# Kernel optimization log

Hardware: AMD Instinct MI355X
Metric: run time of the kernel (lower is better)

## Reference

```python
import math
import jax, jax.numpy as jnp
import numpy as np

EMBED = 1024
INTERNAL = 1024  # EMBED // downsample_rate(=1)
HEADS = 16


def setup_inputs() -> dict:
    key = jax.random.key(0)
    ks = jax.random.split(key, 11)
    b, n, m = 2, 2048, 2048
    s = 1.0 / math.sqrt(EMBED)
    inp = {
        "q": jax.random.normal(ks[0], (b, n, EMBED), jnp.float32),
        "k": jax.random.normal(ks[1], (b, m, EMBED), jnp.float32),
        "v": jax.random.normal(ks[2], (b, m, EMBED), jnp.float32),
        # Linear params (torch Linear: y = x @ W.T + b); store as [in, out].
        "Wq": jax.random.normal(ks[3], (EMBED, INTERNAL), jnp.float32) * s,
        "bq": jax.random.normal(ks[4], (INTERNAL,), jnp.float32) * s,
        "Wk": jax.random.normal(ks[5], (EMBED, INTERNAL), jnp.float32) * s,
        "bk": jax.random.normal(ks[6], (INTERNAL,), jnp.float32) * s,
        "Wv": jax.random.normal(ks[7], (EMBED, INTERNAL), jnp.float32) * s,
        "bv": jax.random.normal(ks[8], (INTERNAL,), jnp.float32) * s,
        "Wo": jax.random.normal(ks[9], (INTERNAL, EMBED), jnp.float32) * s,
        "bo": jax.random.normal(ks[10], (EMBED,), jnp.float32) * s,
    }
    return inp


def _split_heads(x):  # [b, n, c] -> [b, h, n, c/h]
    b, n, c = x.shape
    return x.reshape(b, n, HEADS, c // HEADS).transpose(0, 2, 1, 3)


def reference(q, k, v, Wq, bq, Wk, bk, Wv, bv, Wo, bo):
    qh = _split_heads(q @ Wq + bq)
    kh = _split_heads(k @ Wk + bk)
    vh = _split_heads(v @ Wv + bv)
    c_per_head = kh.shape[-1]
    attn = jnp.einsum("bhnc,bhmc->bhnm", qh, kh) / math.sqrt(c_per_head)
    attn = jax.nn.softmax(attn, axis=-1)
    out = jnp.einsum("bhnm,bhmc->bhnc", attn, vh)
    b, h, n, ch = out.shape
    out = out.transpose(0, 2, 1, 3).reshape(b, n, h * ch)
    return out @ Wo + bo
```

## Files before the change

kernel.cpp:

```cpp
#include <hip/hip_runtime.h>

#define EMBED 1024
#define HEADS 16
#define DHEAD 64
#define BATCH 2
#define SEQ 2048
#define ROWS (BATCH*SEQ)
#define SZA (ROWS*EMBED)
#define SW (EMBED*EMBED)

typedef _Float16 f16;
typedef __attribute__((ext_vector_type(2))) __fp16 h16x2;
typedef __attribute__((ext_vector_type(4))) _Float16 f16x4;
typedef __attribute__((ext_vector_type(8))) _Float16 f16x8;
typedef __attribute__((ext_vector_type(4))) float f32x4;

__device__ __forceinline__ void gld16(const f16* g, f16* lds) {
  __builtin_amdgcn_global_load_lds(
      (const __attribute__((address_space(1))) void*)g,
      (__attribute__((address_space(3))) void*)lds, 16, 0, 0);
}

__global__ __launch_bounds__(256) void pre_kernel(
    const float* __restrict__ q, const float* __restrict__ k,
    const float* __restrict__ v, f16* __restrict__ qc,
    f16* __restrict__ kc, f16* __restrict__ vc,
    const float* __restrict__ w0, const float* __restrict__ w1,
    const float* __restrict__ w2, const float* __restrict__ w3,
    f16* __restrict__ o0, f16* __restrict__ o1,
    f16* __restrict__ o2, f16* __restrict__ o3) {
  __shared__ float tile[32][33];
  const int y = blockIdx.y;
  if (y < 3) {
    const float* in = y == 0 ? q : y == 1 ? k : v;
    f16* out       = y == 0 ? qc : y == 1 ? kc : vc;
    int i = blockIdx.x * 256 + threadIdx.x;
    float4 f = ((const float4* __restrict__)in)[i];
    union { f16 h[4]; short4 s4; } u;
    u.h[0] = (f16)f.x; u.h[1] = (f16)f.y; u.h[2] = (f16)f.z; u.h[3] = (f16)f.w;
    ((short4* __restrict__)out)[i] = u.s4;
    return;
  }
  const int x = blockIdx.x;
  const int z = x >> 10, by = (x >> 5) & 31, bx = x & 31;
  const float* in = z == 0 ? w0 : z == 1 ? w1 : z == 2 ? w2 : w3;
  f16* out       = z == 0 ? o0 : z == 1 ? o1 : z == 2 ? o2 : o3;
  int tx = threadIdx.x & 31, ty = threadIdx.x >> 5;
  #pragma unroll
  for (int i = 0; i < 32; i += 8)
    tile[ty + i][tx] = in[(by*32 + ty + i)*EMBED + bx*32 + tx];
  __syncthreads();
  #pragma unroll
  for (int i = 0; i < 32; i += 8)
    out[(bx*32 + ty + i)*EMBED + by*32 + tx] = (f16)tile[tx][ty + i];
}

__global__ __launch_bounds__(256) void gemm3_kernel(
    const f16* __restrict__ qc, const f16* __restrict__ kc, const f16* __restrict__ vc,
    const f16* __restrict__ Wqt, const f16* __restrict__ Wkt, const f16* __restrict__ Wvt,
    const float* __restrict__ bq, const float* __restrict__ bk, const float* __restrict__ bv,
    f16* __restrict__ Qp, f16* __restrict__ Kp, f16* __restrict__ Vtg) {
  __shared__ __align__(16) f16 As[128*32];
  __shared__ __align__(16) f16 Bs[128*32];
  const int z = blockIdx.y;
  const f16 *A, *Bt; const float* bias; f16* C;
  int mbase, nbase, N, biasrow;
  if (z == 0)      { A=qc;  Bt=Wqt; bias=bq; C=Qp;  mbase=(blockIdx.x&31)*128; nbase=(blockIdx.x>>5)*128; N=EMBED; biasrow=0; }
  else if (z == 1) { A=kc;  Bt=Wkt; bias=bk; C=Kp;  mbase=(blockIdx.x&31)*128; nbase=(blockIdx.x>>5)*128; N=EMBED; biasrow=0; }
  else             { A=Wvt; Bt=vc;  bias=bv; C=Vtg; mbase=(blockIdx.x&7)*128;  nbase=(blockIdx.x>>3)*128; N=ROWS;  biasrow=1; }
  const int K = EMBED;
  const int tid = threadIdx.x;
  const int wave = tid >> 6, lane = tid & 63;
  const int lg = lane >> 4, lr = lane & 15;
  const int wm = (wave >> 1) * 64, wn = (wave & 1) * 64;
  const int sr = lane >> 2, sc = (lane & 3) * 8;
  const f16* gA0 = A  + (size_t)(mbase + wave*16 + sr)*K + sc;
  const f16* gA1 = A  + (size_t)(mbase + 64 + wave*16 + sr)*K + sc;
  const f16* gB0 = Bt + (size_t)(nbase + wave*16 + sr)*K + sc;
  const f16* gB1 = Bt + (size_t)(nbase + 64 + wave*16 + sr)*K + sc;
  f16* lA0 = &As[(wave*16)*32];
  f16* lA1 = &As[(64 + wave*16)*32];
  f16* lB0 = &Bs[(wave*16)*32];
  f16* lB1 = &Bs[(64 + wave*16)*32];
  f32x4 acc[4][4] = {};
  for (int k0 = 0; k0 < K; k0 += 32) {
    __syncthreads();
    gld16(gA0 + k0, lA0);
    gld16(gA1 + k0, lA1);
    gld16(gB0 + k0, lB0);
    gld16(gB1 + k0, lB1);
    __syncthreads();
    f16x8 af[4], bf[4];
    #pragma unroll
    for (int mt = 0; mt < 4; mt++)
      af[mt] = *(const f16x8*)&As[(wm + mt*16 + lr)*32 + lg*8];
    #pragma unroll
    for (int nt = 0; nt < 4; nt++)
      bf[nt] = *(const f16x8*)&Bs[(wn + nt*16 + lr)*32 + lg*8];
    #pragma unroll
    for (int mt = 0; mt < 4; mt++)
      #pragma unroll
      for (int nt = 0; nt < 4; nt++)
        acc[mt][nt] = __builtin_amdgcn_mfma_f32_16x16x32_f16(af[mt], bf[nt], acc[mt][nt], 0, 0, 0);
  }
  #pragma unroll
  for (int mt = 0; mt < 4; mt++)
    #pragma unroll
    for (int nt = 0; nt < 4; nt++)
      #pragma unroll
      for (int i = 0; i < 4; i++) {
        int row = mbase + wm + mt*16 + lg*4 + i;
        int col = nbase + wn + nt*16 + lr;
        float val = acc[mt][nt][i] + (biasrow ? bias[row] : bias[col]);
        C[(size_t)row*N + col] = (f16)val;
      }
}

__global__ __launch_bounds__(256) void gemmo_kernel(
    const f16* __restrict__ A, const f16* __restrict__ Bt,
    const float* __restrict__ bias, float* __restrict__ Cf) {
  __shared__ __align__(16) f16 As[128*32];
  __shared__ __align__(16) f16 Bs[64*32];
  const int K = EMBED, N = EMBED;
  const int tid = threadIdx.x;
  const int wave = tid >> 6, lane = tid & 63;
  const int lg = lane >> 4, lr = lane & 15;
  const int mbase = blockIdx.x * 128, nbase = blockIdx.y * 64;
  const int wm = (wave >> 1) * 64, wn = (wave & 1) * 32;
  const int sr = wave*16 + (lane >> 2), sc = (lane & 3) * 8;
  const f16* gA0 = A  + (size_t)(mbase + sr)*K + sc;
  const f16* gA1 = A  + (size_t)(mbase + 64 + sr)*K + sc;
  const f16* gB  = Bt + (size_t)(nbase + sr)*K + sc;
  f16* lA0 = &As[(wave*16)*32];
  f16* lA1 = &As[(64 + wave*16)*32];
  f16* lB  = &Bs[(wave*16)*32];
  f32x4 acc[4][2] = {};
  for (int k0 = 0; k0 < K; k0 += 32) {
    __syncthreads();
    gld16(gA0 + k0, lA0);
    gld16(gA1 + k0, lA1);
    gld16(gB  + k0, lB);
    __syncthreads();
    f16x8 af[4], bf[2];
    #pragma unroll
    for (int mt = 0; mt < 4; mt++)
      af[mt] = *(const f16x8*)&As[(wm + mt*16 + lr)*32 + lg*8];
    #pragma unroll
    for (int nt = 0; nt < 2; nt++)
      bf[nt] = *(const f16x8*)&Bs[(wn + nt*16 + lr)*32 + lg*8];
    #pragma unroll
    for (int mt = 0; mt < 4; mt++)
      #pragma unroll
      for (int nt = 0; nt < 2; nt++)
        acc[mt][nt] = __builtin_amdgcn_mfma_f32_16x16x32_f16(af[mt], bf[nt], acc[mt][nt], 0, 0, 0);
  }
  #pragma unroll
  for (int mt = 0; mt < 4; mt++)
    #pragma unroll
    for (int nt = 0; nt < 2; nt++)
      #pragma unroll
      for (int i = 0; i < 4; i++) {
        int row = mbase + wm + mt*16 + lg*4 + i;
        int col = nbase + wn + nt*16 + lr;
        Cf[(size_t)row*N + col] = acc[mt][nt][i] + bias[col];
      }
}

__global__ __launch_bounds__(256, 2) void attn_kernel(
    const f16* __restrict__ Qp, const f16* __restrict__ Kp,
    const f16* __restrict__ Vt, f16* __restrict__ Ob) {
  __shared__ __align__(16) f16 Ks[4096];
  __shared__ __align__(16) f16 Vs[4096];
  const int tid = threadIdx.x;
  const int wave = tid >> 6, lane = tid & 63;
  const int lg = lane >> 4, lr = lane & 15;
  const int gid = blockIdx.x;
  const int bh  = (gid & 7)*4 + ((gid >> 3) & 3);
  const int qblk = gid >> 5;
  const int h = bh & 15, b = bh >> 4;
  const int q0 = qblk*128 + wave*32;
  const f16* Qh = Qp + (size_t)b*SEQ*EMBED + h*DHEAD;
  const f16* Kh = Kp + (size_t)b*SEQ*EMBED + h*DHEAD;
  const f16* Vh = Vt + (size_t)h*DHEAD*ROWS + (size_t)b*SEQ;

  const f16* kst[2]; const f16* vst[2]; f16* kdst[2]; f16* vdst[2];
  #pragma unroll
  for (int m = 0; m < 2; m++) {
    int sgrp = m*4 + wave;
    int srow = sgrp*8 + (lane >> 3);
    int sch  = (lane & 7) ^ (srow & 7);
    int prow = ((srow>>5)&1)*32 + ((srow>>4)&1)*4 + ((srow>>2)&3)*8 + (srow&3);
    kst[m] = Kh + (size_t)prow*EMBED + sch*8;
    vst[m] = Vh + (size_t)srow*ROWS + sch*8;
    kdst[m] = &Ks[sgrp*512];
    vdst[m] = &Vs[sgrp*512];
  }

  f16x8 qf[2][2];
  #pragma unroll
  for (int qb = 0; qb < 2; qb++)
    #pragma unroll
    for (int ds = 0; ds < 2; ds++)
      qf[qb][ds] = *(const f16x8*)&Qh[(size_t)(q0 + qb*16 + lr)*EMBED + ds*32 + lg*8];

  const int c0 = ((lg)     ^ (lr & 7)) * 8;
  const int c1 = ((4 + lg) ^ (lr & 7)) * 8;

  f32x4 o[4][2] = {};
  float ls[2] = {};
  const float SC = 0.18033688011f;

  for (int kt = 0; kt < SEQ; kt += 64) {
    __syncthreads();
    gld16(kst[0] + (size_t)kt*EMBED, kdst[0]);
    gld16(kst[1] + (size_t)kt*EMBED, kdst[1]);
    gld16(vst[0] + kt, vdst[0]);
    gld16(vst[1] + kt, vdst[1]);
    __syncthreads();

    f16x8 ka[4][2];
    #pragma unroll
    for (int nb = 0; nb < 4; nb++) {
      ka[nb][0] = *(const f16x8*)&Ks[(nb*16 + lr)*64 + c0];
      ka[nb][1] = *(const f16x8*)&Ks[(nb*16 + lr)*64 + c1];
    }
    f32x4 sa[2][4];
    #pragma unroll
    for (int nb = 0; nb < 4; nb++)
      #pragma unroll
      for (int qb = 0; qb < 2; qb++) {
        f32x4 z = {0.f, 0.f, 0.f, 0.f};
        z = __builtin_amdgcn_mfma_f32_16x16x32_f16(ka[nb][0], qf[qb][0], z, 0, 0, 0);
        z = __builtin_amdgcn_mfma_f32_16x16x32_f16(ka[nb][1], qf[qb][1], z, 0, 0, 0);
        sa[qb][nb] = z;
      }

    f16x8 va[4][2];
    #pragma unroll
    for (int dm = 0; dm < 4; dm++) {
      va[dm][0] = *(const f16x8*)&Vs[(dm*16 + lr)*64 + c0];
      va[dm][1] = *(const f16x8*)&Vs[(dm*16 + lr)*64 + c1];
    }

    f16x8 pf[2][2];
    #pragma unroll
    for (int qb = 0; qb < 2; qb++) {
      float p[4][4];
      #pragma unroll
      for (int nb = 0; nb < 4; nb++)
        #pragma unroll
        for (int i = 0; i < 4; i++) {
          p[nb][i] = __builtin_amdgcn_exp2f(sa[qb][nb][i]*SC - 8.0f);
          ls[qb] += p[nb][i];
        }
      union { f16x8 v; h16x2 h2[4]; } u0, u1;
      u0.h2[0] = __builtin_amdgcn_cvt_pkrtz(p[0][0], p[0][1]);
      u0.h2[1] = __builtin_amdgcn_cvt_pkrtz(p[0][2], p[0][3]);
      u0.h2[2] = __builtin_amdgcn_cvt_pkrtz(p[1][0], p[1][1]);
      u0.h2[3] = __builtin_amdgcn_cvt_pkrtz(p[1][2], p[1][3]);
      u1.h2[0] = __builtin_amdgcn_cvt_pkrtz(p[2][0], p[2][1]);
      u1.h2[1] = __builtin_amdgcn_cvt_pkrtz(p[2][2], p[2][3]);
      u1.h2[2] = __builtin_amdgcn_cvt_pkrtz(p[3][0], p[3][1]);
      u1.h2[3] = __builtin_amdgcn_cvt_pkrtz(p[3][2], p[3][3]);
      pf[qb][0] = u0.v;
      pf[qb][1] = u1.v;
    }

    #pragma unroll
    for (int ks = 0; ks < 2; ks++)
      #pragma unroll
      for (int qb = 0; qb < 2; qb++)
        #pragma unroll
        for (int dm = 0; dm < 4; dm++)
          o[dm][qb] = __builtin_amdgcn_mfma_f32_16x16x32_f16(va[dm][ks], pf[qb][ks], o[dm][qb], 0, 0, 0);
  }

  float inv[2];
  #pragma unroll
  for (int qb = 0; qb < 2; qb++) {
    float s = ls[qb];
    s += __shfl_xor(s, 16);
    s += __shfl_xor(s, 32);
    inv[qb] = 1.f / s;
  }

  #pragma unroll
  for (int qb = 0; qb < 2; qb++) {
    const size_t rowb = (size_t)(b*SEQ + q0 + qb*16 + lr)*EMBED + h*DHEAD;
    #pragma unroll
    for (int dm = 0; dm < 4; dm++) {
      f16x4 w;
      #pragma unroll
      for (int i = 0; i < 4; i++) w[i] = (f16)(o[dm][qb][i] * inv[qb]);
      *(f16x4*)&Ob[rowb + dm*16 + 4*lg] = w;
    }
  }
}

extern "C" void kernel_launch(void* const* d_in, const int* in_sizes, int n_in,
                              void* d_out, int out_size, void* d_ws, size_t ws_size,
                              hipStream_t stream) {
  (void)in_sizes; (void)n_in; (void)out_size; (void)ws_size;
  const float* q  = (const float*)d_in[0];
  const float* k  = (const float*)d_in[1];
  const float* v  = (const float*)d_in[2];
  const float* Wq = (const float*)d_in[3];
  const float* bq = (const float*)d_in[4];
  const float* Wk = (const float*)d_in[5];
  const float* bk = (const float*)d_in[6];
  const float* Wv = (const float*)d_in[7];
  const float* bv = (const float*)d_in[8];
  const float* Wo = (const float*)d_in[9];
  const float* bo = (const float*)d_in[10];
  float* out = (float*)d_out;

  f16* w   = (f16*)d_ws;
  f16* qc  = w;
  f16* kc  = qc + SZA;
  f16* vc  = kc + SZA;
  f16* Qp  = vc + SZA;
  f16* Kp  = Qp + SZA;
  f16* Vtg = Kp + SZA;
  f16* Ob  = Vtg + SZA;
  f16* Wqt = Ob + SZA;
  f16* Wkt = Wqt + SW;
  f16* Wvt = Wkt + SW;
  f16* Wot = Wvt + SW;

  dim3 pg(4096, 4);
  pre_kernel<<<pg, 256, 0, stream>>>(q, k, v, qc, kc, vc,
                                     Wq, Wk, Wv, Wo, Wqt, Wkt, Wvt, Wot);
  dim3 g3(256, 3);
  gemm3_kernel<<<g3, 256, 0, stream>>>(qc, kc, vc, Wqt, Wkt, Wvt, bq, bk, bv, Qp, Kp, Vtg);
  attn_kernel<<<512, 256, 0, stream>>>(Qp, Kp, Vtg, Ob);
  dim3 go(ROWS/128, EMBED/64);
  gemmo_kernel<<<go, 256, 0, stream>>>(Ob, Wot, bo, out);
}
```

Measured before the change: 222.9 us.

## Double-buffer LDS tiles in projection GEMMs and attention loop

Adds two LDS buffers to the QKV GEMM, the output GEMM and the attention K/V loop. The next tile is prefetched with global_load_lds into the spare buffer while MFMAs run on the current one, and the loop now needs one barrier per iteration instead of two. This is meant to hide global-memory latency behind compute. In exchange it doubles LDS use per block, which may lower occupancy, and the last iteration issues a harmless wrap-around prefetch.

```diff
diff --git a/kernel.cpp b/kernel.cpp
--- a/kernel.cpp
+++ b/kernel.cpp
@@ -60,8 +60,8 @@
     const f16* __restrict__ Wqt, const f16* __restrict__ Wkt, const f16* __restrict__ Wvt,
     const float* __restrict__ bq, const float* __restrict__ bk, const float* __restrict__ bv,
     f16* __restrict__ Qp, f16* __restrict__ Kp, f16* __restrict__ Vtg) {
-  __shared__ __align__(16) f16 As[128*32];
-  __shared__ __align__(16) f16 Bs[128*32];
+  __shared__ __align__(16) f16 As[2][128*32];
+  __shared__ __align__(16) f16 Bs[2][128*32];
   const int z = blockIdx.y;
   const f16 *A, *Bt; const float* bias; f16* C;
   int mbase, nbase, N, biasrow;
@@ -78,25 +78,27 @@
   const f16* gA1 = A  + (size_t)(mbase + 64 + wave*16 + sr)*K + sc;
   const f16* gB0 = Bt + (size_t)(nbase + wave*16 + sr)*K + sc;
   const f16* gB1 = Bt + (size_t)(nbase + 64 + wave*16 + sr)*K + sc;
-  f16* lA0 = &As[(wave*16)*32];
-  f16* lA1 = &As[(64 + wave*16)*32];
-  f16* lB0 = &Bs[(wave*16)*32];
-  f16* lB1 = &Bs[(64 + wave*16)*32];
+  const int lo0 = (wave*16)*32, lo1 = (64 + wave*16)*32;
   f32x4 acc[4][4] = {};
-  for (int k0 = 0; k0 < K; k0 += 32) {
+  gld16(gA0, &As[0][lo0]);
+  gld16(gA1, &As[0][lo1]);
+  gld16(gB0, &Bs[0][lo0]);
+  gld16(gB1, &Bs[0][lo1]);
+  for (int it = 0; it < K/32; it++) {
     __syncthreads();
-    gld16(gA0 + k0, lA0);
-    gld16(gA1 + k0, lA1);
-    gld16(gB0 + k0, lB0);
-    gld16(gB1 + k0, lB1);
-    __syncthreads();
+    const int cb = it & 1, nb2 = cb ^ 1;
+    const int kn = ((it + 1) & (K/32 - 1)) * 32;
+    gld16(gA0 + kn, &As[nb2][lo0]);
+    gld16(gA1 + kn, &As[nb2][lo1]);
+    gld16(gB0 + kn, &Bs[nb2][lo0]);
+    gld16(gB1 + kn, &Bs[nb2][lo1]);
     f16x8 af[4], bf[4];
     #pragma unroll
     for (int mt = 0; mt < 4; mt++)
-      af[mt] = *(const f16x8*)&As[(wm + mt*16 + lr)*32 + lg*8];
+      af[mt] = *(const f16x8*)&As[cb][(wm + mt*16 + lr)*32 + lg*8];
     #pragma unroll
     for (int nt = 0; nt < 4; nt++)
-      bf[nt] = *(const f16x8*)&Bs[(wn + nt*16 + lr)*32 + lg*8];
+      bf[nt] = *(const f16x8*)&Bs[cb][(wn + nt*16 + lr)*32 + lg*8];
     #pragma unroll
     for (int mt = 0; mt < 4; mt++)
       #pragma unroll
@@ -119,8 +121,8 @@
 __global__ __launch_bounds__(256) void gemmo_kernel(
     const f16* __restrict__ A, const f16* __restrict__ Bt,
     const float* __restrict__ bias, float* __restrict__ Cf) {
-  __shared__ __align__(16) f16 As[128*32];
-  __shared__ __align__(16) f16 Bs[64*32];
+  __shared__ __align__(16) f16 As[2][128*32];
+  __shared__ __align__(16) f16 Bs[2][64*32];
   const int K = EMBED, N = EMBED;
   const int tid = threadIdx.x;
   const int wave = tid >> 6, lane = tid & 63;
@@ -131,23 +133,25 @@
   const f16* gA0 = A  + (size_t)(mbase + sr)*K + sc;
   const f16* gA1 = A  + (size_t)(mbase + 64 + sr)*K + sc;
   const f16* gB  = Bt + (size_t)(nbase + sr)*K + sc;
-  f16* lA0 = &As[(wave*16)*32];
-  f16* lA1 = &As[(64 + wave*16)*32];
-  f16* lB  = &Bs[(wave*16)*32];
+  const int lo0 = (wave*16)*32, lo1 = (64 + wave*16)*32;
   f32x4 acc[4][2] = {};
-  for (int k0 = 0; k0 < K; k0 += 32) {
+  gld16(gA0, &As[0][lo0]);
+  gld16(gA1, &As[0][lo1]);
+  gld16(gB,  &Bs[0][lo0]);
+  for (int it = 0; it < K/32; it++) {
     __syncthreads();
-    gld16(gA0 + k0, lA0);
-    gld16(gA1 + k0, lA1);
-    gld16(gB  + k0, lB);
-    __syncthreads();
+    const int cb = it & 1, nb2 = cb ^ 1;
+    const int kn = ((it + 1) & (K/32 - 1)) * 32;
+    gld16(gA0 + kn, &As[nb2][lo0]);
+    gld16(gA1 + kn, &As[nb2][lo1]);
+    gld16(gB  + kn, &Bs[nb2][lo0]);
     f16x8 af[4], bf[2];
     #pragma unroll
     for (int mt = 0; mt < 4; mt++)
-      af[mt] = *(const f16x8*)&As[(wm + mt*16 + lr)*32 + lg*8];
+      af[mt] = *(const f16x8*)&As[cb][(wm + mt*16 + lr)*32 + lg*8];
     #pragma unroll
     for (int nt = 0; nt < 2; nt++)
-      bf[nt] = *(const f16x8*)&Bs[(wn + nt*16 + lr)*32 + lg*8];
+      bf[nt] = *(const f16x8*)&Bs[cb][(wn + nt*16 + lr)*32 + lg*8];
     #pragma unroll
     for (int mt = 0; mt < 4; mt++)
       #pragma unroll
@@ -169,8 +173,8 @@
 __global__ __launch_bounds__(256, 2) void attn_kernel(
     const f16* __restrict__ Qp, const f16* __restrict__ Kp,
     const f16* __restrict__ Vt, f16* __restrict__ Ob) {
-  __shared__ __align__(16) f16 Ks[4096];
-  __shared__ __align__(16) f16 Vs[4096];
+  __shared__ __align__(16) f16 Ks[2][4096];
+  __shared__ __align__(16) f16 Vs[2][4096];
   const int tid = threadIdx.x;
   const int wave = tid >> 6, lane = tid & 63;
   const int lg = lane >> 4, lr = lane & 15;
@@ -183,7 +187,7 @@
   const f16* Kh = Kp + (size_t)b*SEQ*EMBED + h*DHEAD;
   const f16* Vh = Vt + (size_t)h*DHEAD*ROWS + (size_t)b*SEQ;
 
-  const f16* kst[2]; const f16* vst[2]; f16* kdst[2]; f16* vdst[2];
+  const f16* kst[2]; const f16* vst[2]; int dsto[2];
   #pragma unroll
   for (int m = 0; m < 2; m++) {
     int sgrp = m*4 + wave;
@@ -192,8 +196,7 @@
     int prow = ((srow>>5)&1)*32 + ((srow>>4)&1)*4 + ((srow>>2)&3)*8 + (srow&3);
     kst[m] = Kh + (size_t)prow*EMBED + sch*8;
     vst[m] = Vh + (size_t)srow*ROWS + sch*8;
-    kdst[m] = &Ks[sgrp*512];
-    vdst[m] = &Vs[sgrp*512];
+    dsto[m] = sgrp*512;
   }
 
   f16x8 qf[2][2];
@@ -210,19 +213,25 @@
   float ls[2] = {};
   const float SC = 0.18033688011f;
 
-  for (int kt = 0; kt < SEQ; kt += 64) {
+  gld16(kst[0], &Ks[0][dsto[0]]);
+  gld16(kst[1], &Ks[0][dsto[1]]);
+  gld16(vst[0], &Vs[0][dsto[0]]);
+  gld16(vst[1], &Vs[0][dsto[1]]);
+
+  for (int t = 0; t < 32; t++) {
     __syncthreads();
-    gld16(kst[0] + (size_t)kt*EMBED, kdst[0]);
-    gld16(kst[1] + (size_t)kt*EMBED, kdst[1]);
-    gld16(vst[0] + kt, vdst[0]);
-    gld16(vst[1] + kt, vdst[1]);
-    __syncthreads();
+    const int cb = t & 1, nb2 = cb ^ 1;
+    const int ktn = ((t + 1) & 31) * 64;
+    gld16(kst[0] + (size_t)ktn*EMBED, &Ks[nb2][dsto[0]]);
+    gld16(kst[1] + (size_t)ktn*EMBED, &Ks[nb2][dsto[1]]);
+    gld16(vst[0] + ktn, &Vs[nb2][dsto[0]]);
+    gld16(vst[1] + ktn, &Vs[nb2][dsto[1]]);
 
     f16x8 ka[4][2];
     #pragma unroll
     for (int nb = 0; nb < 4; nb++) {
-      ka[nb][0] = *(const f16x8*)&Ks[(nb*16 + lr)*64 + c0];
-      ka[nb][1] = *(const f16x8*)&Ks[(nb*16 + lr)*64 + c1];
+      ka[nb][0] = *(const f16x8*)&Ks[cb][(nb*16 + lr)*64 + c0];
+      ka[nb][1] = *(const f16x8*)&Ks[cb][(nb*16 + lr)*64 + c1];
     }
     f32x4 sa[2][4];
     #pragma unroll
@@ -238,8 +247,8 @@
     f16x8 va[4][2];
     #pragma unroll
     for (int dm = 0; dm < 4; dm++) {
-      va[dm][0] = *(const f16x8*)&Vs[(dm*16 + lr)*64 + c0];
-      va[dm][1] = *(const f16x8*)&Vs[(dm*16 + lr)*64 + c1];
+      va[dm][0] = *(const f16x8*)&Vs[cb][(dm*16 + lr)*64 + c0];
+      va[dm][1] = *(const f16x8*)&Vs[cb][(dm*16 + lr)*64 + c1];
     }
 
     f16x8 pf[2][2];
```

New measurement: 225.6 us. About the same (+1.2%).
